# Performance work log

Measured on AMD Instinct MI355X. Metric: run time of the kernel, lower is better.

## Reference

```python
import jax, jax.numpy as jnp
import numpy as np

DIM = 768
HEADS = 12
HEAD_DIM = DIM // HEADS
SCALE = HEAD_DIM ** -0.5


def setup_inputs() -> dict:
    key = jax.random.key(0)
    k1, k2, k3, k4 = jax.random.split(key, 4)
    x = jax.random.normal(k1, (1, 4096, DIM), dtype=jnp.float32)
    # qkv: Linear(dim, 3*dim), bias=False
    W_qkv = jax.random.normal(k2, (DIM, 3 * DIM), dtype=jnp.float32) * (DIM ** -0.5)
    # proj: Linear(dim, dim) with bias
    W_proj = jax.random.normal(k3, (DIM, DIM), dtype=jnp.float32) * (DIM ** -0.5)
    b_proj = jax.random.normal(k4, (DIM,), dtype=jnp.float32) * 0.01
    return {"x": x, "W_qkv": W_qkv, "W_proj": W_proj, "b_proj": b_proj}


def reference(x, W_qkv, W_proj, b_proj):
    b, n, d = x.shape
    qkv = x @ W_qkv                                  # [b, n, 3d]
    q, k, v = jnp.split(qkv, 3, axis=-1)             # each [b, n, d]
    # split heads: [b, n, (h hd)] -> [b, h, n, hd]
    def heads(t):
        return t.reshape(b, n, HEADS, HEAD_DIM).transpose(0, 2, 1, 3)
    q, k, v = heads(q) * SCALE, heads(k), heads(v)
    sim = jnp.einsum('bhid,bhjd->bhij', q, k)        # [b, h, n, n] -- full score matrix
    attn = jax.nn.softmax(sim, axis=-1)
    out = jnp.einsum('bhij,bhjd->bhid', attn, v)     # [b, h, n, hd]
    out = out.transpose(0, 2, 1, 3).reshape(b, n, d)  # merge heads
    return out @ W_proj + b_proj
```

## Files before the change

kernel.cpp:

```cpp
#include <hip/hip_runtime.h>
#include <math.h>

#define TOKENS 4096
#define DMODEL 768
#define NHEADS 12
#define HDIM   64
#define QKV_N  2304
#define ATTN_SCALE 0.125f
#define QSCALE_LOG2E (0.125f * 1.44269504088896340736f)

typedef __attribute__((ext_vector_type(8))) short bf16x8;
typedef __attribute__((ext_vector_type(4))) float floatx4;

__device__ __forceinline__ ushort f2bf(float f) {
    union { float f; unsigned u; } cv; cv.f = f;
    unsigned u = cv.u;
    u += 0x7fffu + ((u >> 16) & 1u);
    return (ushort)(u >> 16);
}

__device__ __forceinline__ unsigned cvt_pk_bf16(float a, float b) {
    unsigned r;
    asm("v_cvt_pk_bf16_f32 %0, %1, %2" : "=v"(r) : "v"(a), "v"(b));
    return r;
}

__device__ __forceinline__ void gl2lds16(const ushort* g, ushort* l) {
    __builtin_amdgcn_global_load_lds(
        (const __attribute__((address_space(1))) void*)g,
        (__attribute__((address_space(3))) void*)l, 16, 0, 0);
}

__device__ __forceinline__ bf16x8 frag(const ushort* ls, int row, int chunk) {
    return *(const bf16x8*)(ls + row * 64 + ((chunk ^ (row & 7)) * 8));
}

__global__ __launch_bounds__(256) void cvt_bf16_kernel(
    const float* __restrict__ in, ushort* __restrict__ out, int n4)
{
    const int i = blockIdx.x * 256 + threadIdx.x;
    if (i < n4) {
        const float4 v = ((const float4*)in)[i];
        ushort4 h;
        h.x = f2bf(v.x); h.y = f2bf(v.y); h.z = f2bf(v.z); h.w = f2bf(v.w);
        ((ushort4*)out)[i] = h;
    }
}

__global__ __launch_bounds__(256) void transpose_cvt_kernel(
    const float* __restrict__ in, ushort* __restrict__ out, int R, int C)
{
    __shared__ ushort tile[32][33];
    const int tx  = threadIdx.x & 31;
    const int ty8 = threadIdx.x >> 5;
    const int c0 = blockIdx.x * 32;
    const int r0 = blockIdx.y * 32;
    #pragma unroll
    for (int p = 0; p < 4; ++p) {
        const int r = ty8 + p * 8;
        tile[r][tx] = f2bf(in[(size_t)(r0 + r) * C + c0 + tx]);
    }
    __syncthreads();
    #pragma unroll
    for (int p = 0; p < 4; ++p) {
        const int c = ty8 + p * 8;
        out[(size_t)(c0 + c) * R + r0 + tx] = tile[tx][c];
    }
}

template<int NT>
__device__ __forceinline__ void gemm_body_async(
    const ushort* __restrict__ A, const ushort* __restrict__ Bt, int K,
    int m0, int n0, floatx4 acc[4][NT], ushort* ls)
{
    ushort* lsA = ls;
    ushort* lsB = ls + 8192;

    const int tid  = threadIdx.x;
    const int lane = tid & 63;
    const int wave = tid >> 6;
    const int wm = wave >> 1, wn = wave & 1;
    const int quad = lane >> 4, l16 = lane & 15;

    const int lrow = lane >> 3;
    const int csw  = ((lane & 7) ^ lrow) * 8;

    const ushort* gA = A  + (size_t)(m0 + wave * 32 + lrow) * K + csw;
    const ushort* gB = Bt + (size_t)(n0 + wave * NT * 8 + lrow) * K + csw;
    ushort* lA = lsA + (wave * 32) * 64;
    ushort* lB = lsB + (wave * NT * 8) * 64;

    for (int k0 = 0; k0 < K; k0 += 64) {
        __syncthreads();
        #pragma unroll
        for (int p = 0; p < 4; ++p)
            gl2lds16(gA + (size_t)p * 8 * K + k0, lA + p * 8 * 64);
        #pragma unroll
        for (int p = 0; p < NT; ++p)
            gl2lds16(gB + (size_t)p * 8 * K + k0, lB + p * 8 * 64);
        __syncthreads();

        #pragma unroll
        for (int ks = 0; ks < 2; ++ks) {
            bf16x8 af[4], bfr[NT];
            #pragma unroll
            for (int mt = 0; mt < 4; ++mt)
                af[mt] = frag(lsA, wm * 64 + mt * 16 + l16, ks * 4 + quad);
            #pragma unroll
            for (int nt = 0; nt < NT; ++nt)
                bfr[nt] = frag(lsB, wn * NT * 16 + nt * 16 + l16, ks * 4 + quad);
            #pragma unroll
            for (int mt = 0; mt < 4; ++mt)
                #pragma unroll
                for (int nt = 0; nt < NT; ++nt)
                    acc[mt][nt] = __builtin_amdgcn_mfma_f32_16x16x32_bf16(
                        af[mt], bfr[nt], acc[mt][nt], 0, 0, 0);
        }
    }
}

__global__ __launch_bounds__(256) void gemm_qkv_mfma(
    const ushort* __restrict__ Xb, const ushort* __restrict__ Wt,
    ushort* __restrict__ Qb, ushort* __restrict__ Kb, ushort* __restrict__ Vt)
{
    __shared__ __align__(16) ushort ls[16384];
    const int m0 = blockIdx.y * 128;
    const int n0 = blockIdx.x * 128;

    floatx4 acc[4][4] = {};
    gemm_body_async<4>(Xb, Wt, DMODEL, m0, n0, acc, ls);

    const int tid  = threadIdx.x;
    const int lane = tid & 63;
    const int wave = tid >> 6;
    const int wm = wave >> 1, wn = wave & 1;
    const int quad = lane >> 4, l16 = lane & 15;

    if (n0 < 2 * DMODEL) {
        const float scale = (n0 < DMODEL) ? QSCALE_LOG2E : 1.0f;
        ushort* outp = (n0 < DMODEL) ? Qb : Kb;
        const int colg = (n0 < DMODEL) ? n0 : n0 - DMODEL;
        #pragma unroll
        for (int p = 0; p < 2; ++p) {
            __syncthreads();
            if (wm == p) {
                #pragma unroll
                for (int mt = 0; mt < 4; ++mt)
                    #pragma unroll
                    for (int nt = 0; nt < 4; ++nt) {
                        const int row = mt * 16 + quad * 4;
                        const int col = wn * 64 + nt * 16 + l16;
                        #pragma unroll
                        for (int r = 0; r < 4; ++r)
                            ls[(row + r) * 136 + col] = f2bf(acc[mt][nt][r] * scale);
                    }
            }
            __syncthreads();
            #pragma unroll
            for (int p2 = 0; p2 < 4; ++p2) {
                const int row = (tid >> 4) + p2 * 16;
                const int c8  = (tid & 15) * 8;
                *(uint4*)(outp + (size_t)(m0 + p * 64 + row) * DMODEL + colg + c8) =
                    *(const uint4*)(ls + row * 136 + c8);
            }
        }
    } else {
        const int hd0 = n0 - 2 * DMODEL;
        #pragma unroll
        for (int p = 0; p < 2; ++p) {
            __syncthreads();
            if (wn == p) {
                #pragma unroll
                for (int mt = 0; mt < 4; ++mt)
                    #pragma unroll
                    for (int nt = 0; nt < 4; ++nt) {
                        const int hd  = nt * 16 + l16;
                        const int tok = wm * 64 + mt * 16 + quad * 4;
                        #pragma unroll
                        for (int r = 0; r < 4; ++r)
                            ls[hd * 136 + tok + r] = f2bf(acc[mt][nt][r]);
                    }
            }
            __syncthreads();
            #pragma unroll
            for (int p2 = 0; p2 < 4; ++p2) {
                const int row = (tid >> 4) + p2 * 16;
                const int c8  = (tid & 15) * 8;
                *(uint4*)(Vt + (size_t)(hd0 + p * 64 + row) * TOKENS + m0 + c8) =
                    *(const uint4*)(ls + row * 136 + c8);
            }
        }
    }
}

__global__ __launch_bounds__(256) void gemm_proj_mfma(
    const ushort* __restrict__ Ab, const ushort* __restrict__ Wt,
    const float* __restrict__ bias, float* __restrict__ out)
{
    __shared__ __align__(16) ushort ls[12288];
    const int m0 = blockIdx.y * 128;
    const int n0 = blockIdx.x * 64;

    floatx4 acc[4][2] = {};
    gemm_body_async<2>(Ab, Wt, DMODEL, m0, n0, acc, ls);

    const int lane = threadIdx.x & 63;
    const int wave = threadIdx.x >> 6;
    const int wm = wave >> 1, wn = wave & 1;
    const int quad = lane >> 4, l16 = lane & 15;
    const int row0 = m0 + wm * 64 + quad * 4;
    const int col0 = n0 + wn * 32;

    #pragma unroll
    for (int nt = 0; nt < 2; ++nt) {
        const int col = col0 + nt * 16 + l16;
        const float bv = bias[col];
        #pragma unroll
        for (int mt = 0; mt < 4; ++mt)
            #pragma unroll
            for (int r = 0; r < 4; ++r)
                out[(size_t)(row0 + mt * 16 + r) * DMODEL + col] =
                    acc[mt][nt][r] + bv;
    }
}

__global__ __launch_bounds__(256, 2) void attn_mfma_kernel(
    const ushort* __restrict__ Qb, const ushort* __restrict__ Kb,
    const ushort* __restrict__ Vt, ushort* __restrict__ attn_out)
{
    __shared__ __align__(16) ushort lds[32768];

    const int tid  = threadIdx.x;
    const int wave = tid >> 6;
    const int lane = tid & 63;
    const int quad = lane >> 4;
    const int l16  = lane & 15;
    const int h    = blockIdx.y;
    const int i0   = blockIdx.x * 64;

    bf16x8 qf[4][2];
    #pragma unroll
    for (int jt = 0; jt < 4; ++jt) {
        const ushort* qb = Qb + (size_t)(i0 + jt * 16 + l16) * DMODEL + h * HDIM;
        qf[jt][0] = *(const bf16x8*)(qb + quad * 8);
        qf[jt][1] = *(const bf16x8*)(qb + 32 + quad * 8);
    }

    bf16x8 ones;
    #pragma unroll
    for (int i = 0; i < 8; ++i) ones[i] = (short)0x3F80;

    floatx4 O[4][4] = {};
    floatx4 Ol[4]   = {};

    ushort* wls = lds + wave * 8192;

    const int lrow8 = lane >> 3;
    const int csw8  = ((lane & 7) ^ lrow8) * 8;
    const ushort* gK = Kb + (size_t)(wave * 32 + lrow8) * DMODEL + h * HDIM + csw8;

    const int vrow4 = lane >> 2;
    const int vslot = (lane & 3) ^ (vrow4 & 3);
    const ushort* gV = Vt + (size_t)(h * HDIM + vrow4) * TOKENS + wave * 32 + vslot * 8;

    const int vx = l16 & 3;
    const int vo0 = (((quad >> 1)    ) ^ vx) * 8 + (quad & 1) * 4;
    const int vo1 = ((2 + (quad >> 1)) ^ vx) * 8 + (quad & 1) * 4;

    #pragma unroll
    for (int p = 0; p < 4; ++p)
        gl2lds16(gK + (size_t)p * 8 * DMODEL, wls + p * 512);
    #pragma unroll
    for (int p = 0; p < 4; ++p)
        gl2lds16(gV + (size_t)p * 16 * TOKENS, wls + 2048 + p * 512);

    for (int t = 0; t < TOKENS / 128; ++t) {
        const int cur = t & 1;
        const ushort* Kc = wls + cur * 4096;
        const ushort* Vc = Kc + 2048;

        if (t < TOKENS / 128 - 1) {
            ushort* Kn = wls + (1 - cur) * 4096;
            const size_t jn = (size_t)(t + 1) * 128;
            #pragma unroll
            for (int p = 0; p < 4; ++p)
                gl2lds16(gK + (jn + p * 8) * DMODEL, Kn + p * 512);
            #pragma unroll
            for (int p = 0; p < 4; ++p)
                gl2lds16(gV + (size_t)p * 16 * TOKENS + jn, Kn + 2048 + p * 512);
            asm volatile("s_waitcnt vmcnt(8)" ::: "memory");
        } else {
            asm volatile("s_waitcnt vmcnt(0)" ::: "memory");
        }
        __builtin_amdgcn_sched_barrier(0);

        bf16x8 af[2][2];
        #pragma unroll
        for (int kt2 = 0; kt2 < 2; ++kt2)
            #pragma unroll
            for (int kh = 0; kh < 2; ++kh)
                af[kt2][kh] = frag(Kc, kt2 * 16 + l16, kh * 4 + quad);

        bf16x8 vf[4];
        #pragma unroll
        for (int nt = 0; nt < 4; ++nt) {
            const ushort* vb = Vc + (nt * 16 + l16) * 32;
            union { bf16x8 v; uint2 d[2]; } vu;
            vu.d[0] = *(const uint2*)(vb + vo0);
            vu.d[1] = *(const uint2*)(vb + vo1);
            vf[nt] = vu.v;
        }

        floatx4 Sv[4][2];
        __builtin_amdgcn_s_setprio(1);
        #pragma unroll
        for (int jt = 0; jt < 4; ++jt)
            #pragma unroll
            for (int kt2 = 0; kt2 < 2; ++kt2) {
                floatx4 s = {0.f, 0.f, 0.f, 0.f};
                s = __builtin_amdgcn_mfma_f32_16x16x32_bf16(af[kt2][0], qf[jt][0], s, 0, 0, 0);
                s = __builtin_amdgcn_mfma_f32_16x16x32_bf16(af[kt2][1], qf[jt][1], s, 0, 0, 0);
                Sv[jt][kt2] = s;
            }
        __builtin_amdgcn_s_setprio(0);

        bf16x8 pa[4];
        #pragma unroll
        for (int jt = 0; jt < 4; ++jt) {
            union { bf16x8 v; unsigned u[4]; } pu;
            #pragma unroll
            for (int kt2 = 0; kt2 < 2; ++kt2) {
                const float p0 = __builtin_amdgcn_exp2f(Sv[jt][kt2][0]);
                const float p1 = __builtin_amdgcn_exp2f(Sv[jt][kt2][1]);
                const float p2 = __builtin_amdgcn_exp2f(Sv[jt][kt2][2]);
                const float p3 = __builtin_amdgcn_exp2f(Sv[jt][kt2][3]);
                pu.u[kt2 * 2]     = cvt_pk_bf16(p0, p1);
                pu.u[kt2 * 2 + 1] = cvt_pk_bf16(p2, p3);
            }
            pa[jt] = pu.v;
            Ol[jt] = __builtin_amdgcn_mfma_f32_16x16x32_bf16(pa[jt], ones, Ol[jt], 0, 0, 0);
        }

        __builtin_amdgcn_s_setprio(1);
        #pragma unroll
        for (int jt = 0; jt < 4; ++jt)
            #pragma unroll
            for (int nt = 0; nt < 4; ++nt)
                O[jt][nt] = __builtin_amdgcn_mfma_f32_16x16x32_bf16(
                    pa[jt], vf[nt], O[jt][nt], 0, 0, 0);
        __builtin_amdgcn_s_setprio(0);
    }

    __syncthreads();
    float* Of  = (float*)lds;
    float* Olf = ((float*)lds) + 3 * 64 * 66;
    if (wave != 0) {
        const int rg = (wave - 1) * 64 * 66;
        #pragma unroll
        for (int jt = 0; jt < 4; ++jt) {
            #pragma unroll
            for (int nt = 0; nt < 4; ++nt)
                #pragma unroll
                for (int r = 0; r < 4; ++r)
                    Of[rg + (jt * 16 + quad * 4 + r) * 66 + nt * 16 + l16] = O[jt][nt][r];
            if (l16 == 0) {
                #pragma unroll
                for (int r = 0; r < 4; ++r)
                    Olf[(wave - 1) * 64 + jt * 16 + quad * 4 + r] = Ol[jt][r];
            }
        }
    }
    __syncthreads();
    if (wave == 0) {
        #pragma unroll
        for (int jt = 0; jt < 4; ++jt) {
            const int qr = jt * 16 + quad * 4;
            float linv[4];
            #pragma unroll
            for (int r = 0; r < 4; ++r) {
                const float l = Ol[jt][r] + Olf[qr + r] + Olf[64 + qr + r]
                              + Olf[128 + qr + r];
                linv[r] = __builtin_amdgcn_rcpf(l);
            }
            #pragma unroll
            for (int nt = 0; nt < 4; ++nt) {
                const int d = h * HDIM + nt * 16 + l16;
                #pragma unroll
                for (int r = 0; r < 4; ++r) {
                    const float o = O[jt][nt][r]
                        + Of[(qr + r) * 66 + nt * 16 + l16]
                        + Of[64 * 66 + (qr + r) * 66 + nt * 16 + l16]
                        + Of[2 * 64 * 66 + (qr + r) * 66 + nt * 16 + l16];
                    attn_out[(size_t)(i0 + qr + r) * DMODEL + d] = f2bf(o * linv[r]);
                }
            }
        }
    }
}

extern "C" void kernel_launch(void* const* d_in, const int* in_sizes, int n_in,
                              void* d_out, int out_size, void* d_ws, size_t ws_size,
                              hipStream_t stream)
{
    const float* x     = (const float*)d_in[0];
    const float* Wqkv  = (const float*)d_in[1];
    const float* Wproj = (const float*)d_in[2];
    const float* bproj = (const float*)d_in[3];
    float* out = (float*)d_out;

    ushort* Xb     = (ushort*)d_ws;
    ushort* WqkvT  = Xb    + (size_t)TOKENS * DMODEL;
    ushort* WprojT = WqkvT + (size_t)QKV_N * DMODEL;
    ushort* Qb     = WprojT + (size_t)DMODEL * DMODEL;
    ushort* Kb     = Qb    + (size_t)TOKENS * DMODEL;
    ushort* Vt     = Kb    + (size_t)TOKENS * DMODEL;
    ushort* attn   = Vt    + (size_t)TOKENS * DMODEL;

    cvt_bf16_kernel<<<dim3(TOKENS * DMODEL / 4 / 256), 256, 0, stream>>>(
        x, Xb, TOKENS * DMODEL / 4);
    transpose_cvt_kernel<<<dim3(QKV_N / 32, DMODEL / 32), 256, 0, stream>>>(
        Wqkv, WqkvT, DMODEL, QKV_N);
    transpose_cvt_kernel<<<dim3(DMODEL / 32, DMODEL / 32), 256, 0, stream>>>(
        Wproj, WprojT, DMODEL, DMODEL);

    gemm_qkv_mfma<<<dim3(QKV_N / 128, TOKENS / 128), 256, 0, stream>>>(
        Xb, WqkvT, Qb, Kb, Vt);

    attn_mfma_kernel<<<dim3(TOKENS / 64, NHEADS), 256, 0, stream>>>(
        Qb, Kb, Vt, attn);

    gemm_proj_mfma<<<dim3(DMODEL / 64, TOKENS / 128), 256, 0, stream>>>(
        attn, WprojT, bproj, out);
}
```

Before: 208.3 us.

## Shrink attention LDS staging to 16-key sub-tiles and raise occupancy to three blocks

The attention kernel now stages K and V in 16-row sub-tiles per wave, with a finer-grained double/quad buffer, instead of 32-row tiles. This cuts per-block LDS from 64KB to about 50KB, so launch bounds can request three blocks per CU. Score computation, exp and bf16 packing are interleaved per half-tile, which shrinks live score registers to help fit the tighter register budget. The risks are more waitcnt synchronisation points per key and possible register spills under the higher occupancy bound.

```diff
diff --git a/kernel.cpp b/kernel.cpp
--- a/kernel.cpp
+++ b/kernel.cpp
@@ -224,11 +224,11 @@
     }
 }
 
-__global__ __launch_bounds__(256, 2) void attn_mfma_kernel(
+__global__ __launch_bounds__(256, 3) void attn_mfma_kernel(
     const ushort* __restrict__ Qb, const ushort* __restrict__ Kb,
     const ushort* __restrict__ Vt, ushort* __restrict__ attn_out)
 {
-    __shared__ __align__(16) ushort lds[32768];
+    __shared__ __align__(16) ushort lds[25728];
 
     const int tid  = threadIdx.x;
     const int wave = tid >> 6;
@@ -253,101 +253,104 @@
     floatx4 O[4][4] = {};
     floatx4 Ol[4]   = {};
 
-    ushort* wls = lds + wave * 8192;
+    ushort* wls = lds + wave * 6144;
 
     const int lrow8 = lane >> 3;
     const int csw8  = ((lane & 7) ^ lrow8) * 8;
-    const ushort* gK = Kb + (size_t)(wave * 32 + lrow8) * DMODEL + h * HDIM + csw8;
-
-    const int vrow4 = lane >> 2;
-    const int vslot = (lane & 3) ^ (vrow4 & 3);
-    const ushort* gV = Vt + (size_t)(h * HDIM + vrow4) * TOKENS + wave * 32 + vslot * 8;
-
-    const int vx = l16 & 3;
-    const int vo0 = (((quad >> 1)    ) ^ vx) * 8 + (quad & 1) * 4;
-    const int vo1 = ((2 + (quad >> 1)) ^ vx) * 8 + (quad & 1) * 4;
-
-    #pragma unroll
-    for (int p = 0; p < 4; ++p)
-        gl2lds16(gK + (size_t)p * 8 * DMODEL, wls + p * 512);
-    #pragma unroll
-    for (int p = 0; p < 4; ++p)
-        gl2lds16(gV + (size_t)p * 16 * TOKENS, wls + 2048 + p * 512);
-
-    for (int t = 0; t < TOKENS / 128; ++t) {
-        const int cur = t & 1;
-        const ushort* Kc = wls + cur * 4096;
-        const ushort* Vc = Kc + 2048;
-
-        if (t < TOKENS / 128 - 1) {
-            ushort* Kn = wls + (1 - cur) * 4096;
-            const size_t jn = (size_t)(t + 1) * 128;
-            #pragma unroll
-            for (int p = 0; p < 4; ++p)
-                gl2lds16(gK + (jn + p * 8) * DMODEL, Kn + p * 512);
-            #pragma unroll
-            for (int p = 0; p < 4; ++p)
-                gl2lds16(gV + (size_t)p * 16 * TOKENS + jn, Kn + 2048 + p * 512);
-            asm volatile("s_waitcnt vmcnt(8)" ::: "memory");
+    const ushort* gK0 = Kb + (size_t)(wave * 16 + lrow8) * DMODEL + h * HDIM + csw8;
+    const ushort* gK1 = gK0 + (size_t)8 * DMODEL;
+
+    const ushort* gV0 = Vt + (size_t)(h * HDIM + (lane >> 1)) * TOKENS
+                           + wave * 16 + (lane & 1) * 8;
+    const ushort* gV1 = gV0 + (size_t)32 * TOKENS;
+
+    union { bf16x8 v; unsigned u[4]; } pa[4];
+
+    gl2lds16(gK0, wls);
+    gl2lds16(gK1, wls + 512);
+    gl2lds16(gV0, wls + 2048);
+    gl2lds16(gV1, wls + 2048 + 512);
+
+    for (int u = 0; u < 32; ++u) {
+        const int s0 = (u & 1) << 1;
+        ushort* Kc0 = wls;
+        ushort* Kc1 = wls + 1024;
+        ushort* V0  = wls + 2048 + s0 * 1024;
+        ushort* V1  = wls + 2048 + (s0 + 1) * 1024;
+        ushort* Vn  = wls + 2048 + ((s0 + 2) & 3) * 1024;
+
+        {
+            const size_t t1 = (size_t)(2 * u + 1) * 64;
+            gl2lds16(gK0 + t1 * DMODEL, Kc1);
+            gl2lds16(gK1 + t1 * DMODEL, Kc1 + 512);
+            gl2lds16(gV0 + t1, V1);
+            gl2lds16(gV1 + t1, V1 + 512);
+        }
+        asm volatile("s_waitcnt vmcnt(4)" ::: "memory");
+        __builtin_amdgcn_sched_barrier(0);
+
+        {
+            const bf16x8 a0 = frag(Kc0, l16, quad);
+            const bf16x8 a1 = frag(Kc0, l16, 4 + quad);
+            __builtin_amdgcn_s_setprio(1);
+            #pragma unroll
+            for (int jt = 0; jt < 4; ++jt) {
+                floatx4 s = {0.f, 0.f, 0.f, 0.f};
+                s = __builtin_amdgcn_mfma_f32_16x16x32_bf16(a0, qf[jt][0], s, 0, 0, 0);
+                s = __builtin_amdgcn_mfma_f32_16x16x32_bf16(a1, qf[jt][1], s, 0, 0, 0);
+                pa[jt].u[0] = cvt_pk_bf16(__builtin_amdgcn_exp2f(s[0]),
+                                          __builtin_amdgcn_exp2f(s[1]));
+                pa[jt].u[1] = cvt_pk_bf16(__builtin_amdgcn_exp2f(s[2]),
+                                          __builtin_amdgcn_exp2f(s[3]));
+            }
+            __builtin_amdgcn_s_setprio(0);
+        }
+
+        if (u < 31) {
+            const size_t t2 = (size_t)(2 * u + 2) * 64;
+            gl2lds16(gK0 + t2 * DMODEL, Kc0);
+            gl2lds16(gK1 + t2 * DMODEL, Kc0 + 512);
+            gl2lds16(gV0 + t2, Vn);
+            gl2lds16(gV1 + t2, Vn + 512);
+            asm volatile("s_waitcnt vmcnt(4)" ::: "memory");
         } else {
             asm volatile("s_waitcnt vmcnt(0)" ::: "memory");
         }
         __builtin_amdgcn_sched_barrier(0);
 
-        bf16x8 af[2][2];
-        #pragma unroll
-        for (int kt2 = 0; kt2 < 2; ++kt2)
-            #pragma unroll
-            for (int kh = 0; kh < 2; ++kh)
-                af[kt2][kh] = frag(Kc, kt2 * 16 + l16, kh * 4 + quad);
-
-        bf16x8 vf[4];
+        {
+            const bf16x8 a0 = frag(Kc1, l16, quad);
+            const bf16x8 a1 = frag(Kc1, l16, 4 + quad);
+            __builtin_amdgcn_s_setprio(1);
+            #pragma unroll
+            for (int jt = 0; jt < 4; ++jt) {
+                floatx4 s = {0.f, 0.f, 0.f, 0.f};
+                s = __builtin_amdgcn_mfma_f32_16x16x32_bf16(a0, qf[jt][0], s, 0, 0, 0);
+                s = __builtin_amdgcn_mfma_f32_16x16x32_bf16(a1, qf[jt][1], s, 0, 0, 0);
+                pa[jt].u[2] = cvt_pk_bf16(__builtin_amdgcn_exp2f(s[0]),
+                                          __builtin_amdgcn_exp2f(s[1]));
+                pa[jt].u[3] = cvt_pk_bf16(__builtin_amdgcn_exp2f(s[2]),
+                                          __builtin_amdgcn_exp2f(s[3]));
+            }
+            __builtin_amdgcn_s_setprio(0);
+        }
+
+        __builtin_amdgcn_s_setprio(1);
         #pragma unroll
         for (int nt = 0; nt < 4; ++nt) {
-            const ushort* vb = Vc + (nt * 16 + l16) * 32;
+            const int ro = (nt * 16 + l16) * 16 + quad * 4;
             union { bf16x8 v; uint2 d[2]; } vu;
-            vu.d[0] = *(const uint2*)(vb + vo0);
-            vu.d[1] = *(const uint2*)(vb + vo1);
-            vf[nt] = vu.v;
-        }
-
-        floatx4 Sv[4][2];
-        __builtin_amdgcn_s_setprio(1);
+            vu.d[0] = *(const uint2*)(V0 + ro);
+            vu.d[1] = *(const uint2*)(V1 + ro);
+            #pragma unroll
+            for (int jt = 0; jt < 4; ++jt)
+                O[jt][nt] = __builtin_amdgcn_mfma_f32_16x16x32_bf16(
+                    pa[jt].v, vu.v, O[jt][nt], 0, 0, 0);
+        }
         #pragma unroll
         for (int jt = 0; jt < 4; ++jt)
-            #pragma unroll
-            for (int kt2 = 0; kt2 < 2; ++kt2) {
-                floatx4 s = {0.f, 0.f, 0.f, 0.f};
-                s = __builtin_amdgcn_mfma_f32_16x16x32_bf16(af[kt2][0], qf[jt][0], s, 0, 0, 0);
-                s = __builtin_amdgcn_mfma_f32_16x16x32_bf16(af[kt2][1], qf[jt][1], s, 0, 0, 0);
-                Sv[jt][kt2] = s;
-            }
-        __builtin_amdgcn_s_setprio(0);
-
-        bf16x8 pa[4];
-        #pragma unroll
-        for (int jt = 0; jt < 4; ++jt) {
-            union { bf16x8 v; unsigned u[4]; } pu;
-            #pragma unroll
-            for (int kt2 = 0; kt2 < 2; ++kt2) {
-                const float p0 = __builtin_amdgcn_exp2f(Sv[jt][kt2][0]);
-                const float p1 = __builtin_amdgcn_exp2f(Sv[jt][kt2][1]);
-                const float p2 = __builtin_amdgcn_exp2f(Sv[jt][kt2][2]);
-                const float p3 = __builtin_amdgcn_exp2f(Sv[jt][kt2][3]);
-                pu.u[kt2 * 2]     = cvt_pk_bf16(p0, p1);
-                pu.u[kt2 * 2 + 1] = cvt_pk_bf16(p2, p3);
-            }
-            pa[jt] = pu.v;
-            Ol[jt] = __builtin_amdgcn_mfma_f32_16x16x32_bf16(pa[jt], ones, Ol[jt], 0, 0, 0);
-        }
-
-        __builtin_amdgcn_s_setprio(1);
-        #pragma unroll
-        for (int jt = 0; jt < 4; ++jt)
-            #pragma unroll
-            for (int nt = 0; nt < 4; ++nt)
-                O[jt][nt] = __builtin_amdgcn_mfma_f32_16x16x32_bf16(
-                    pa[jt], vf[nt], O[jt][nt], 0, 0, 0);
+            Ol[jt] = __builtin_amdgcn_mfma_f32_16x16x32_bf16(
+                pa[jt].v, ones, Ol[jt], 0, 0, 0);
         __builtin_amdgcn_s_setprio(0);
     }
 
```

After: 202.2 us. 1.03x faster.
